# Optimization experiments

Measured on AMD Instinct MI355X. Metric: run time of the kernel, lower is better.

The kernel has to match this reference:

```python
import jax, jax.numpy as jnp
import numpy as np

B, H, SQ, SKV, D = 2, 16, 2048, 2048, 64
SCALE = 8  # sqrt(head_dim)


def setup_inputs() -> dict:
    key = jax.random.key(0)
    kq, kk, kv, km = jax.random.split(key, 4)
    q = jax.random.normal(kq, (B, H, SQ, D), dtype=jnp.float32)
    k = jax.random.normal(kk, (B, H, SKV, D), dtype=jnp.float32)
    v = jax.random.normal(kv, (B, H, SKV, D), dtype=jnp.float32)
    mask = jax.random.normal(km, (1, 1, SQ, SKV), dtype=jnp.float32)
    return {"q": q, "k": k, "v": v, "mask": mask, "scale": SCALE}


def reference(q, k, v, mask, scale):
    # scores: [B, H, SQ, SKV]
    scores = jnp.einsum("bhqd,bhkd->bhqk", q, k) / scale
    scores = scores + mask  # broadcast additive mask
    probs = jax.nn.softmax(scores, axis=-1)
    # hidden: [B, H, SQ, D]
    return jnp.einsum("bhqk,bhkd->bhqd", probs, v)
```

## Files before the change

kernel.cpp:

```cpp
#include <hip/hip_runtime.h>
#include <hip/hip_bf16.h>

#define NB 2
#define NH 16
#define NSQ 2048
#define NSKV 2048
#define ND 64
#define NT (NSKV / 64)
#define LOG2E 1.4426950408889634f

typedef __attribute__((ext_vector_type(8))) short bf16x8;
typedef __attribute__((ext_vector_type(4))) float f32x4;

__device__ __forceinline__ short f2bf(float x) {
  union { float f; unsigned u; } c; c.f = x;
  unsigned r = c.u + 0x7fffu + ((c.u >> 16) & 1u);
  return (short)(r >> 16);
}
__device__ __forceinline__ unsigned pack_bf2(float lo, float hi) {
  union { __hip_bfloat162 h; unsigned u; } c;
  c.h = __float22bfloat162_rn(float2{lo, hi});
  return c.u;
}
__device__ __forceinline__ float u2f(unsigned u) {
  union { unsigned u; float f; } c; c.u = u; return c.f;
}
__device__ __forceinline__ float exp2_fast(float x) {
#if __has_builtin(__builtin_amdgcn_exp2f)
  return __builtin_amdgcn_exp2f(x);
#else
  return exp2f(x);
#endif
}

__device__ __forceinline__ int kvmap(int x) {
  return (x & 3) | (((x >> 4) & 1) << 2) | (((x >> 2) & 1) << 3)
       | (((x >> 3) & 1) << 4) | (x & 32);
}

__global__ void prep_k(const float* __restrict__ K, short* __restrict__ Kp) {
  const int bh   = blockIdx.y;
  const int t    = (int)threadIdx.x;
  const int rout = blockIdx.x * 16 + (t >> 4);
  const int c    = (t & 15) * 4;
  const int rsrc = (rout & ~63) | kvmap(rout & 63);
  float4 v = *(const float4*)(K + ((size_t)bh * NSKV + rsrc) * ND + c);
  short4 o;
  o.x = f2bf(v.x); o.y = f2bf(v.y); o.z = f2bf(v.z); o.w = f2bf(v.w);
  *(short4*)(Kp + ((size_t)bh * NSKV + rout) * ND + c) = o;
}

__global__ void prep_vt(const float* __restrict__ V, short* __restrict__ Vt) {
  __shared__ float T[64][65];
  const int kv0 = blockIdx.x * 64;
  const int bh  = blockIdx.y;
  const int t   = (int)threadIdx.x;
  const float* src = V + ((size_t)bh * NSKV + kv0) * ND;
#pragma unroll
  for (int i = 0; i < 4; ++i) {
    float4 v = *(const float4*)(src + (size_t)((t >> 4) + 16 * i) * ND + (t & 15) * 4);
    T[(t >> 4) + 16 * i][(t & 15) * 4 + 0] = v.x;
    T[(t >> 4) + 16 * i][(t & 15) * 4 + 1] = v.y;
    T[(t >> 4) + 16 * i][(t & 15) * 4 + 2] = v.z;
    T[(t >> 4) + 16 * i][(t & 15) * 4 + 3] = v.w;
  }
  __syncthreads();
  const int d = t >> 2, kc = (t & 3) * 16;
  short* dst = Vt + ((size_t)bh * ND + d) * NSKV + kv0 + kc;
  bf16x8 w0, w1;
#pragma unroll
  for (int j = 0; j < 8; ++j) w0[j] = f2bf(T[kc + j][d]);
#pragma unroll
  for (int j = 0; j < 8; ++j) w1[j] = f2bf(T[kc + 8 + j][d]);
  *(bf16x8*)dst = w0;
  *(bf16x8*)(dst + 8) = w1;
}

__global__ void prep_mt(const float* __restrict__ M, unsigned short* __restrict__ Mt) {
  const int qt = blockIdx.x;
  const int kt = blockIdx.y;
  const int t  = (int)threadIdx.x;
  const int rl = t >> 4;
  const int c  = t & 15;
  const int row = qt * 16 + rl;
  float4 v = *(const float4*)(M + (size_t)row * NSKV + kt * 64 + c * 4);
  const int nt   = 2 * (c >> 3) + (c & 1);
  const int lq   = (c >> 1) & 3;
  const int lane = lq * 16 + rl;
  ushort4 o;
  o.x = (unsigned short)f2bf(LOG2E * v.x);
  o.y = (unsigned short)f2bf(LOG2E * v.y);
  o.z = (unsigned short)f2bf(LOG2E * v.z);
  o.w = (unsigned short)f2bf(LOG2E * v.w);
  *(ushort4*)(Mt + (((size_t)qt * 32 + kt) * 64 + lane) * 16 + nt * 4) = o;
}

__global__ __launch_bounds__(256, 2)
void attn_fwd(const float* __restrict__ Q, const short* __restrict__ Kbf,
              const short* __restrict__ Vt, const unsigned short* __restrict__ Mt,
              const void* __restrict__ scale_p, float* __restrict__ O)
{
  const int lin = (int)blockIdx.x + ((int)blockIdx.y << 4);
  const int swz = ((lin & 7) << 6) | (lin >> 3);
  const int qb  = swz & 15;
  const int bh  = swz >> 4;

  const int tid = (int)threadIdx.x;
  const int wv  = tid >> 6;
  const int ln  = tid & 63;
  const int l16 = ln & 15;
  const int lq  = ln >> 4;

  float scale_v;
  {
    union { int i; float f; } u;
    u.i = ((const int*)scale_p)[0];
    float af = fabsf(u.f);
    scale_v = (af >= 1e-6f && af <= 1e6f) ? u.f : (float)u.i;
  }
  const float qmul = LOG2E / scale_v;

  const int q0 = qb * 128;
  const short* Kg = Kbf + (size_t)bh * NSKV * ND;
  const short* Vg = Vt  + (size_t)bh * ND * NSKV;

  __shared__ short Kl[2][64][64];
  __shared__ short Vl[2][64][64];

  const int srow0  = tid >> 3;
  const int schunk = tid & 7;

  bf16x8 kst[2], vst[2];
#pragma unroll
  for (int j = 0; j < 2; ++j) {
    const int row = srow0 + j * 32;
    kst[j] = *(const bf16x8*)(Kg + (size_t)row * ND + schunk * 8);
    vst[j] = *(const bf16x8*)(Vg + (size_t)row * NSKV + schunk * 8);
  }

  bf16x8 qf[2][2];
  {
#pragma unroll
    for (int qs = 0; qs < 2; ++qs) {
      const float* qrow = Q + ((size_t)bh * NSQ + q0 + wv * 32 + qs * 16 + l16) * ND;
#pragma unroll
      for (int kc = 0; kc < 2; ++kc) {
        const float4* p = (const float4*)(qrow + kc * 32 + lq * 8);
        float4 a = p[0], b = p[1];
        bf16x8 f;
        f[0]=f2bf(a.x*qmul); f[1]=f2bf(a.y*qmul); f[2]=f2bf(a.z*qmul); f[3]=f2bf(a.w*qmul);
        f[4]=f2bf(b.x*qmul); f[5]=f2bf(b.y*qmul); f[6]=f2bf(b.z*qmul); f[7]=f2bf(b.w*qmul);
        qf[qs][kc] = f;
      }
    }
  }

  f32x4 oa[2][4];
  f32x4 lacc[2];
#pragma unroll
  for (int qs = 0; qs < 2; ++qs) {
#pragma unroll
    for (int dt = 0; dt < 4; ++dt) { f32x4 z = {0.f,0.f,0.f,0.f}; oa[qs][dt] = z; }
    f32x4 z = {0.f,0.f,0.f,0.f}; lacc[qs] = z;
  }

  bf16x8 ones;
#pragma unroll
  for (int j = 0; j < 8; ++j) ones[j] = (short)0x3F80;

  const unsigned short* Mq0 = Mt + ((size_t)(qb * 8 + wv * 2)) * 32 * 64 * 16 + (size_t)ln * 16;
  const unsigned short* Mq1 = Mq0 + (size_t)32 * 64 * 16;

  auto lds_write = [&](int buf) {
#pragma unroll
    for (int j = 0; j < 2; ++j) {
      const int row  = srow0 + j * 32;
      const int slot = schunk ^ (row & 7);
      *(bf16x8*)&Kl[buf][row][slot * 8] = kst[j];
      *(bf16x8*)&Vl[buf][row][slot * 8] = vst[j];
    }
  };

  union MU { uint4 q[2]; unsigned u[8]; };
  MU mc[2];

  lds_write(0);
  mc[0].q[0] = *(const uint4*)(Mq0);
  mc[0].q[1] = *(const uint4*)(Mq0 + 8);
  mc[1].q[0] = *(const uint4*)(Mq1);
  mc[1].q[1] = *(const uint4*)(Mq1 + 8);
  __syncthreads();

  for (int t = 0; t < NT; ++t) {
    const int cur = t & 1;
    const int kvb = t * 64;

    if (t + 1 < NT) {
#pragma unroll
      for (int j = 0; j < 2; ++j) {
        const int row = srow0 + j * 32;
        kst[j] = *(const bf16x8*)(Kg + (size_t)(kvb + 64 + row) * ND + schunk * 8);
        vst[j] = *(const bf16x8*)(Vg + (size_t)row * NSKV + kvb + 64 + schunk * 8);
      }
    }

    bf16x8 kf[4][2];
#pragma unroll
    for (int nt = 0; nt < 4; ++nt)
#pragma unroll
      for (int kc = 0; kc < 2; ++kc) {
        const int row = nt * 16 + l16;
        kf[nt][kc] = *(const bf16x8*)&Kl[cur][row][(((kc << 2) | lq) ^ (row & 7)) * 8];
      }

    f32x4 s0[4], s1[4];
    __builtin_amdgcn_s_setprio(1);
#pragma unroll
    for (int nt = 0; nt < 4; ++nt) {
      f32x4 a0 = {0.f,0.f,0.f,0.f};
      a0 = __builtin_amdgcn_mfma_f32_16x16x32_bf16(kf[nt][0], qf[0][0], a0, 0, 0, 0);
      a0 = __builtin_amdgcn_mfma_f32_16x16x32_bf16(kf[nt][1], qf[0][1], a0, 0, 0, 0);
      s0[nt] = a0;
      f32x4 a1 = {0.f,0.f,0.f,0.f};
      a1 = __builtin_amdgcn_mfma_f32_16x16x32_bf16(kf[nt][0], qf[1][0], a1, 0, 0, 0);
      a1 = __builtin_amdgcn_mfma_f32_16x16x32_bf16(kf[nt][1], qf[1][1], a1, 0, 0, 0);
      s1[nt] = a1;
    }
    __builtin_amdgcn_s_setprio(0);

    bf16x8 vfr[4][2];
#pragma unroll
    for (int dt = 0; dt < 4; ++dt)
#pragma unroll
      for (int kc = 0; kc < 2; ++kc) {
        const int row = dt * 16 + l16;
        vfr[dt][kc] = *(const bf16x8*)&Vl[cur][row][(((kc << 2) | lq) ^ (row & 7)) * 8];
      }

    {
#pragma unroll
      for (int nt = 0; nt < 4; ++nt) {
        const unsigned w0 = mc[0].u[nt * 2], w1 = mc[0].u[nt * 2 + 1];
        s0[nt][0] = exp2_fast(s0[nt][0] + u2f(w0 << 16));
        s0[nt][1] = exp2_fast(s0[nt][1] + u2f(w0 & 0xffff0000u));
        s0[nt][2] = exp2_fast(s0[nt][2] + u2f(w1 << 16));
        s0[nt][3] = exp2_fast(s0[nt][3] + u2f(w1 & 0xffff0000u));
      }
      bf16x8 pa[2];
#pragma unroll
      for (int kc = 0; kc < 2; ++kc) {
        union { unsigned u[4]; bf16x8 v; } w;
        w.u[0] = pack_bf2(s0[2*kc][0],   s0[2*kc][1]);
        w.u[1] = pack_bf2(s0[2*kc][2],   s0[2*kc][3]);
        w.u[2] = pack_bf2(s0[2*kc+1][0], s0[2*kc+1][1]);
        w.u[3] = pack_bf2(s0[2*kc+1][2], s0[2*kc+1][3]);
        pa[kc] = w.v;
      }
      __builtin_amdgcn_s_setprio(1);
#pragma unroll
      for (int kc = 0; kc < 2; ++kc) {
#pragma unroll
        for (int dt = 0; dt < 4; ++dt)
          oa[0][dt] = __builtin_amdgcn_mfma_f32_16x16x32_bf16(pa[kc], vfr[dt][kc], oa[0][dt], 0, 0, 0);
        lacc[0] = __builtin_amdgcn_mfma_f32_16x16x32_bf16(pa[kc], ones, lacc[0], 0, 0, 0);
      }
      __builtin_amdgcn_s_setprio(0);
    }

    {
#pragma unroll
      for (int nt = 0; nt < 4; ++nt) {
        const unsigned w0 = mc[1].u[nt * 2], w1 = mc[1].u[nt * 2 + 1];
        s1[nt][0] = exp2_fast(s1[nt][0] + u2f(w0 << 16));
        s1[nt][1] = exp2_fast(s1[nt][1] + u2f(w0 & 0xffff0000u));
        s1[nt][2] = exp2_fast(s1[nt][2] + u2f(w1 << 16));
        s1[nt][3] = exp2_fast(s1[nt][3] + u2f(w1 & 0xffff0000u));
      }
      if (t + 1 < NT) {
        const unsigned short* mp0 = Mq0 + (size_t)(t + 1) * 64 * 16;
        const unsigned short* mp1 = Mq1 + (size_t)(t + 1) * 64 * 16;
        mc[0].q[0] = *(const uint4*)(mp0);
        mc[0].q[1] = *(const uint4*)(mp0 + 8);
        mc[1].q[0] = *(const uint4*)(mp1);
        mc[1].q[1] = *(const uint4*)(mp1 + 8);
      }
      bf16x8 pa[2];
#pragma unroll
      for (int kc = 0; kc < 2; ++kc) {
        union { unsigned u[4]; bf16x8 v; } w;
        w.u[0] = pack_bf2(s1[2*kc][0],   s1[2*kc][1]);
        w.u[1] = pack_bf2(s1[2*kc][2],   s1[2*kc][3]);
        w.u[2] = pack_bf2(s1[2*kc+1][0], s1[2*kc+1][1]);
        w.u[3] = pack_bf2(s1[2*kc+1][2], s1[2*kc+1][3]);
        pa[kc] = w.v;
      }
      __builtin_amdgcn_s_setprio(1);
#pragma unroll
      for (int kc = 0; kc < 2; ++kc) {
#pragma unroll
        for (int dt = 0; dt < 4; ++dt)
          oa[1][dt] = __builtin_amdgcn_mfma_f32_16x16x32_bf16(pa[kc], vfr[dt][kc], oa[1][dt], 0, 0, 0);
        lacc[1] = __builtin_amdgcn_mfma_f32_16x16x32_bf16(pa[kc], ones, lacc[1], 0, 0, 0);
      }
      __builtin_amdgcn_s_setprio(0);
    }

    if (t + 1 < NT) lds_write(cur ^ 1);
    __syncthreads();
  }

#pragma unroll
  for (int qs = 0; qs < 2; ++qs)
#pragma unroll
    for (int r = 0; r < 4; ++r) {
      const float inv = 1.0f / lacc[qs][r];
      float* orow = O + ((size_t)bh * NSQ + q0 + wv * 32 + qs * 16 + lq * 4 + r) * ND;
#pragma unroll
      for (int dt = 0; dt < 4; ++dt)
        orow[dt * 16 + l16] = oa[qs][dt][r] * inv;
    }
}

extern "C" void kernel_launch(void* const* d_in, const int* in_sizes, int n_in,
                              void* d_out, int out_size, void* d_ws, size_t ws_size,
                              hipStream_t stream) {
  const float* q     = (const float*)d_in[0];
  const float* k     = (const float*)d_in[1];
  const float* v     = (const float*)d_in[2];
  const float* mask  = (const float*)d_in[3];
  const void*  scale = (const void*)d_in[4];
  float* out = (float*)d_out;

  const size_t NELEM = (size_t)NB * NH * NSKV * ND;
  short* Kbf = (short*)d_ws;
  short* Vtp = Kbf + NELEM;
  unsigned short* Mtl = (unsigned short*)(Vtp + NELEM);

  prep_k<<<dim3(NSKV / 16, NB * NH), 256, 0, stream>>>(k, Kbf);
  prep_vt<<<dim3(NSKV / 64, NB * NH), 256, 0, stream>>>(v, Vtp);
  prep_mt<<<dim3(NSQ / 16, NSKV / 64), 256, 0, stream>>>(mask, Mtl);

  dim3 grid(NSQ / 128, NB * NH);
  attn_fwd<<<grid, 256, 0, stream>>>(q, Kbf, Vtp, Mtl, scale, out);
}
```

Before: 73.70 us.

## Pre-pack K/V into MFMA fragment layout and load directly from global, dropping LDS

The prep kernels now write K and V in per-lane MFMA fragment order, so each lane loads its fragments with contiguous 16-byte global reads. This removes LDS staging, the swizzle and the per-tile __syncthreads. K fragments for the next tile are register-prefetched, and the two q-subtile QK/PV phases are interleaved to overlap exp work with MFMA. In exchange, every wave re-reads K/V from global/L2 instead of sharing them through LDS across four waves, and register pressure rises.

Measured after the change: 78.87 us. 1.07x slower.

```diff
diff --git a/kernel.cpp b/kernel.cpp
--- a/kernel.cpp
+++ b/kernel.cpp
@@ -8,6 +8,7 @@
 #define ND 64
 #define NT (NSKV / 64)
 #define LOG2E 1.4426950408889634f
+#define BHSTRIDE (NSKV * ND)
 
 typedef __attribute__((ext_vector_type(8))) short bf16x8;
 typedef __attribute__((ext_vector_type(4))) float f32x4;
@@ -39,18 +40,23 @@
 }
 
 __global__ void prep_k(const float* __restrict__ K, short* __restrict__ Kp) {
-  const int bh   = blockIdx.y;
-  const int t    = (int)threadIdx.x;
-  const int rout = blockIdx.x * 16 + (t >> 4);
-  const int c    = (t & 15) * 4;
-  const int rsrc = (rout & ~63) | kvmap(rout & 63);
-  float4 v = *(const float4*)(K + ((size_t)bh * NSKV + rsrc) * ND + c);
-  short4 o;
-  o.x = f2bf(v.x); o.y = f2bf(v.y); o.z = f2bf(v.z); o.w = f2bf(v.w);
-  *(short4*)(Kp + ((size_t)bh * NSKV + rout) * ND + c) = o;
-}
-
-__global__ void prep_vt(const float* __restrict__ V, short* __restrict__ Vt) {
+  const int bh = blockIdx.y, tile = blockIdx.x, tid = (int)threadIdx.x;
+#pragma unroll
+  for (int h = 0; h < 2; ++h) {
+    const int u    = tid + h * 256;
+    const int nt   = u >> 7, kc = (u >> 6) & 1, lane = u & 63;
+    const int prow = nt * 16 + (lane & 15);
+    const float* src = K + ((size_t)bh * NSKV + tile * 64 + kvmap(prow)) * ND
+                         + kc * 32 + (lane >> 4) * 8;
+    float4 a = *(const float4*)src, b = *(const float4*)(src + 4);
+    bf16x8 w;
+    w[0]=f2bf(a.x); w[1]=f2bf(a.y); w[2]=f2bf(a.z); w[3]=f2bf(a.w);
+    w[4]=f2bf(b.x); w[5]=f2bf(b.y); w[6]=f2bf(b.z); w[7]=f2bf(b.w);
+    *(bf16x8*)(Kp + (size_t)bh * BHSTRIDE + (size_t)tile * 4096 + u * 8) = w;
+  }
+}
+
+__global__ void prep_vt(const float* __restrict__ V, short* __restrict__ Vp) {
   __shared__ float T[64][65];
   const int kv0 = blockIdx.x * 64;
   const int bh  = blockIdx.y;
@@ -65,15 +71,18 @@
     T[(t >> 4) + 16 * i][(t & 15) * 4 + 3] = v.w;
   }
   __syncthreads();
-  const int d = t >> 2, kc = (t & 3) * 16;
-  short* dst = Vt + ((size_t)bh * ND + d) * NSKV + kv0 + kc;
+  const int d = t >> 2, c = t & 3;
   bf16x8 w0, w1;
 #pragma unroll
-  for (int j = 0; j < 8; ++j) w0[j] = f2bf(T[kc + j][d]);
-#pragma unroll
-  for (int j = 0; j < 8; ++j) w1[j] = f2bf(T[kc + 8 + j][d]);
-  *(bf16x8*)dst = w0;
-  *(bf16x8*)(dst + 8) = w1;
+  for (int j = 0; j < 8; ++j) w0[j] = f2bf(T[c * 16 + j][d]);
+#pragma unroll
+  for (int j = 0; j < 8; ++j) w1[j] = f2bf(T[c * 16 + 8 + j][d]);
+  const int frag  = (d >> 4) * 2 + (c >> 1);
+  const int lane0 = (((2 * c) & 3) << 4) | (d & 15);
+  const int lane1 = (((2 * c + 1) & 3) << 4) | (d & 15);
+  short* dstb = Vp + (size_t)bh * BHSTRIDE + (size_t)blockIdx.x * 4096 + frag * 512;
+  *(bf16x8*)(dstb + lane0 * 8) = w0;
+  *(bf16x8*)(dstb + lane1 * 8) = w1;
 }
 
 __global__ void prep_mt(const float* __restrict__ M, unsigned short* __restrict__ Mt) {
@@ -96,8 +105,8 @@
 }
 
 __global__ __launch_bounds__(256, 2)
-void attn_fwd(const float* __restrict__ Q, const short* __restrict__ Kbf,
-              const short* __restrict__ Vt, const unsigned short* __restrict__ Mt,
+void attn_fwd(const float* __restrict__ Q, const short* __restrict__ Kp,
+              const short* __restrict__ Vp, const unsigned short* __restrict__ Mt,
               const void* __restrict__ scale_p, float* __restrict__ O)
 {
   const int lin = (int)blockIdx.x + ((int)blockIdx.y << 4);
@@ -121,37 +130,21 @@
   const float qmul = LOG2E / scale_v;
 
   const int q0 = qb * 128;
-  const short* Kg = Kbf + (size_t)bh * NSKV * ND;
-  const short* Vg = Vt  + (size_t)bh * ND * NSKV;
-
-  __shared__ short Kl[2][64][64];
-  __shared__ short Vl[2][64][64];
-
-  const int srow0  = tid >> 3;
-  const int schunk = tid & 7;
-
-  bf16x8 kst[2], vst[2];
-#pragma unroll
-  for (int j = 0; j < 2; ++j) {
-    const int row = srow0 + j * 32;
-    kst[j] = *(const bf16x8*)(Kg + (size_t)row * ND + schunk * 8);
-    vst[j] = *(const bf16x8*)(Vg + (size_t)row * NSKV + schunk * 8);
-  }
+  const short* Kb = Kp + (size_t)bh * BHSTRIDE;
+  const short* Vb = Vp + (size_t)bh * BHSTRIDE;
 
   bf16x8 qf[2][2];
-  {
-#pragma unroll
-    for (int qs = 0; qs < 2; ++qs) {
-      const float* qrow = Q + ((size_t)bh * NSQ + q0 + wv * 32 + qs * 16 + l16) * ND;
-#pragma unroll
-      for (int kc = 0; kc < 2; ++kc) {
-        const float4* p = (const float4*)(qrow + kc * 32 + lq * 8);
-        float4 a = p[0], b = p[1];
-        bf16x8 f;
-        f[0]=f2bf(a.x*qmul); f[1]=f2bf(a.y*qmul); f[2]=f2bf(a.z*qmul); f[3]=f2bf(a.w*qmul);
-        f[4]=f2bf(b.x*qmul); f[5]=f2bf(b.y*qmul); f[6]=f2bf(b.z*qmul); f[7]=f2bf(b.w*qmul);
-        qf[qs][kc] = f;
-      }
+#pragma unroll
+  for (int qs = 0; qs < 2; ++qs) {
+    const float* qrow = Q + ((size_t)bh * NSQ + q0 + wv * 32 + qs * 16 + l16) * ND;
+#pragma unroll
+    for (int kc = 0; kc < 2; ++kc) {
+      const float4* p = (const float4*)(qrow + kc * 32 + lq * 8);
+      float4 a = p[0], b = p[1];
+      bf16x8 f;
+      f[0]=f2bf(a.x*qmul); f[1]=f2bf(a.y*qmul); f[2]=f2bf(a.z*qmul); f[3]=f2bf(a.w*qmul);
+      f[4]=f2bf(b.x*qmul); f[5]=f2bf(b.y*qmul); f[6]=f2bf(b.z*qmul); f[7]=f2bf(b.w*qmul);
+      qf[qs][kc] = f;
     }
   }
 
@@ -171,72 +164,50 @@
   const unsigned short* Mq0 = Mt + ((size_t)(qb * 8 + wv * 2)) * 32 * 64 * 16 + (size_t)ln * 16;
   const unsigned short* Mq1 = Mq0 + (size_t)32 * 64 * 16;
 
-  auto lds_write = [&](int buf) {
-#pragma unroll
-    for (int j = 0; j < 2; ++j) {
-      const int row  = srow0 + j * 32;
-      const int slot = schunk ^ (row & 7);
-      *(bf16x8*)&Kl[buf][row][slot * 8] = kst[j];
-      *(bf16x8*)&Vl[buf][row][slot * 8] = vst[j];
-    }
-  };
-
   union MU { uint4 q[2]; unsigned u[8]; };
-  MU mc[2];
-
-  lds_write(0);
+  MU mc[2], mn[2];
+
+  bf16x8 kfc[4][2], kfn[4][2], vf[4][2];
+#pragma unroll
+  for (int nt = 0; nt < 4; ++nt)
+#pragma unroll
+    for (int kc = 0; kc < 2; ++kc)
+      kfc[nt][kc] = *(const bf16x8*)(Kb + (nt * 2 + kc) * 512 + ln * 8);
   mc[0].q[0] = *(const uint4*)(Mq0);
   mc[0].q[1] = *(const uint4*)(Mq0 + 8);
   mc[1].q[0] = *(const uint4*)(Mq1);
   mc[1].q[1] = *(const uint4*)(Mq1 + 8);
-  __syncthreads();
-
+
+#pragma unroll 2
   for (int t = 0; t < NT; ++t) {
-    const int cur = t & 1;
-    const int kvb = t * 64;
+    const short* Vt0 = Vb + (size_t)t * 4096;
+#pragma unroll
+    for (int dt = 0; dt < 4; ++dt)
+#pragma unroll
+      for (int kc = 0; kc < 2; ++kc)
+        vf[dt][kc] = *(const bf16x8*)(Vt0 + (dt * 2 + kc) * 512 + ln * 8);
 
     if (t + 1 < NT) {
-#pragma unroll
-      for (int j = 0; j < 2; ++j) {
-        const int row = srow0 + j * 32;
-        kst[j] = *(const bf16x8*)(Kg + (size_t)(kvb + 64 + row) * ND + schunk * 8);
-        vst[j] = *(const bf16x8*)(Vg + (size_t)row * NSKV + kvb + 64 + schunk * 8);
-      }
-    }
-
-    bf16x8 kf[4][2];
-#pragma unroll
-    for (int nt = 0; nt < 4; ++nt)
-#pragma unroll
-      for (int kc = 0; kc < 2; ++kc) {
-        const int row = nt * 16 + l16;
-        kf[nt][kc] = *(const bf16x8*)&Kl[cur][row][(((kc << 2) | lq) ^ (row & 7)) * 8];
-      }
-
-    f32x4 s0[4], s1[4];
+      const short* Kt1 = Kb + (size_t)(t + 1) * 4096;
+#pragma unroll
+      for (int nt = 0; nt < 4; ++nt)
+#pragma unroll
+        for (int kc = 0; kc < 2; ++kc)
+          kfn[nt][kc] = *(const bf16x8*)(Kt1 + (nt * 2 + kc) * 512 + ln * 8);
+    }
+
+    f32x4 s0[4];
     __builtin_amdgcn_s_setprio(1);
 #pragma unroll
     for (int nt = 0; nt < 4; ++nt) {
-      f32x4 a0 = {0.f,0.f,0.f,0.f};
-      a0 = __builtin_amdgcn_mfma_f32_16x16x32_bf16(kf[nt][0], qf[0][0], a0, 0, 0, 0);
-      a0 = __builtin_amdgcn_mfma_f32_16x16x32_bf16(kf[nt][1], qf[0][1], a0, 0, 0, 0);
-      s0[nt] = a0;
-      f32x4 a1 = {0.f,0.f,0.f,0.f};
-      a1 = __builtin_amdgcn_mfma_f32_16x16x32_bf16(kf[nt][0], qf[1][0], a1, 0, 0, 0);
-      a1 = __builtin_amdgcn_mfma_f32_16x16x32_bf16(kf[nt][1], qf[1][1], a1, 0, 0, 0);
-      s1[nt] = a1;
+      f32x4 a = {0.f,0.f,0.f,0.f};
+      a = __builtin_amdgcn_mfma_f32_16x16x32_bf16(kfc[nt][0], qf[0][0], a, 0, 0, 0);
+      a = __builtin_amdgcn_mfma_f32_16x16x32_bf16(kfc[nt][1], qf[0][1], a, 0, 0, 0);
+      s0[nt] = a;
     }
     __builtin_amdgcn_s_setprio(0);
 
-    bf16x8 vfr[4][2];
-#pragma unroll
-    for (int dt = 0; dt < 4; ++dt)
-#pragma unroll
-      for (int kc = 0; kc < 2; ++kc) {
-        const int row = dt * 16 + l16;
-        vfr[dt][kc] = *(const bf16x8*)&Vl[cur][row][(((kc << 2) | lq) ^ (row & 7)) * 8];
-      }
-
+    bf16x8 pa0[2];
     {
 #pragma unroll
       for (int nt = 0; nt < 4; ++nt) {
@@ -246,7 +217,6 @@
         s0[nt][2] = exp2_fast(s0[nt][2] + u2f(w1 << 16));
         s0[nt][3] = exp2_fast(s0[nt][3] + u2f(w1 & 0xffff0000u));
       }
-      bf16x8 pa[2];
 #pragma unroll
       for (int kc = 0; kc < 2; ++kc) {
         union { unsigned u[4]; bf16x8 v; } w;
@@ -254,19 +224,41 @@
         w.u[1] = pack_bf2(s0[2*kc][2],   s0[2*kc][3]);
         w.u[2] = pack_bf2(s0[2*kc+1][0], s0[2*kc+1][1]);
         w.u[3] = pack_bf2(s0[2*kc+1][2], s0[2*kc+1][3]);
-        pa[kc] = w.v;
+        pa0[kc] = w.v;
       }
-      __builtin_amdgcn_s_setprio(1);
-#pragma unroll
-      for (int kc = 0; kc < 2; ++kc) {
-#pragma unroll
-        for (int dt = 0; dt < 4; ++dt)
-          oa[0][dt] = __builtin_amdgcn_mfma_f32_16x16x32_bf16(pa[kc], vfr[dt][kc], oa[0][dt], 0, 0, 0);
-        lacc[0] = __builtin_amdgcn_mfma_f32_16x16x32_bf16(pa[kc], ones, lacc[0], 0, 0, 0);
-      }
-      __builtin_amdgcn_s_setprio(0);
-    }
-
+    }
+
+    f32x4 s1[4];
+    __builtin_amdgcn_s_setprio(1);
+#pragma unroll
+    for (int nt = 0; nt < 4; ++nt) {
+      f32x4 a = {0.f,0.f,0.f,0.f};
+      a = __builtin_amdgcn_mfma_f32_16x16x32_bf16(kfc[nt][0], qf[1][0], a, 0, 0, 0);
+      a = __builtin_amdgcn_mfma_f32_16x16x32_bf16(kfc[nt][1], qf[1][1], a, 0, 0, 0);
+      s1[nt] = a;
+    }
+    __builtin_amdgcn_s_setprio(0);
+
+    if (t + 1 < NT) {
+      const unsigned short* mp0 = Mq0 + (size_t)(t + 1) * 64 * 16;
+      const unsigned short* mp1 = Mq1 + (size_t)(t + 1) * 64 * 16;
+      mn[0].q[0] = *(const uint4*)(mp0);
+      mn[0].q[1] = *(const uint4*)(mp0 + 8);
+      mn[1].q[0] = *(const uint4*)(mp1);
+      mn[1].q[1] = *(const uint4*)(mp1 + 8);
+    }
+
+    __builtin_amdgcn_s_setprio(1);
+#pragma unroll
+    for (int kc = 0; kc < 2; ++kc) {
+#pragma unroll
+      for (int dt = 0; dt < 4; ++dt)
+        oa[0][dt] = __builtin_amdgcn_mfma_f32_16x16x32_bf16(pa0[kc], vf[dt][kc], oa[0][dt], 0, 0, 0);
+      lacc[0] = __builtin_amdgcn_mfma_f32_16x16x32_bf16(pa0[kc], ones, lacc[0], 0, 0, 0);
+    }
+    __builtin_amdgcn_s_setprio(0);
+
+    bf16x8 pa1[2];
     {
 #pragma unroll
       for (int nt = 0; nt < 4; ++nt) {
@@ -276,15 +268,6 @@
         s1[nt][2] = exp2_fast(s1[nt][2] + u2f(w1 << 16));
         s1[nt][3] = exp2_fast(s1[nt][3] + u2f(w1 & 0xffff0000u));
       }
-      if (t + 1 < NT) {
-        const unsigned short* mp0 = Mq0 + (size_t)(t + 1) * 64 * 16;
-        const unsigned short* mp1 = Mq1 + (size_t)(t + 1) * 64 * 16;
-        mc[0].q[0] = *(const uint4*)(mp0);
-        mc[0].q[1] = *(const uint4*)(mp0 + 8);
-        mc[1].q[0] = *(const uint4*)(mp1);
-        mc[1].q[1] = *(const uint4*)(mp1 + 8);
-      }
-      bf16x8 pa[2];
 #pragma unroll
       for (int kc = 0; kc < 2; ++kc) {
         union { unsigned u[4]; bf16x8 v; } w;
@@ -292,21 +275,27 @@
         w.u[1] = pack_bf2(s1[2*kc][2],   s1[2*kc][3]);
         w.u[2] = pack_bf2(s1[2*kc+1][0], s1[2*kc+1][1]);
         w.u[3] = pack_bf2(s1[2*kc+1][2], s1[2*kc+1][3]);
-        pa[kc] = w.v;
+        pa1[kc] = w.v;
       }
-      __builtin_amdgcn_s_setprio(1);
-#pragma unroll
-      for (int kc = 0; kc < 2; ++kc) {
-#pragma unroll
-        for (int dt = 0; dt < 4; ++dt)
-          oa[1][dt] = __builtin_amdgcn_mfma_f32_16x16x32_bf16(pa[kc], vfr[dt][kc], oa[1][dt], 0, 0, 0);
-        lacc[1] = __builtin_amdgcn_mfma_f32_16x16x32_bf16(pa[kc], ones, lacc[1], 0, 0, 0);
-      }
-      __builtin_amdgcn_s_setprio(0);
-    }
-
-    if (t + 1 < NT) lds_write(cur ^ 1);
-    __syncthreads();
+    }
+
+    __builtin_amdgcn_s_setprio(1);
+#pragma unroll
+    for (int kc = 0; kc < 2; ++kc) {
+#pragma unroll
+      for (int dt = 0; dt < 4; ++dt)
+        oa[1][dt] = __builtin_amdgcn_mfma_f32_16x16x32_bf16(pa1[kc], vf[dt][kc], oa[1][dt], 0, 0, 0);
+      lacc[1] = __builtin_amdgcn_mfma_f32_16x16x32_bf16(pa1[kc], ones, lacc[1], 0, 0, 0);
+    }
+    __builtin_amdgcn_s_setprio(0);
+
+#pragma unroll
+    for (int nt = 0; nt < 4; ++nt)
+#pragma unroll
+      for (int kc = 0; kc < 2; ++kc)
+        kfc[nt][kc] = kfn[nt][kc];
+    mc[0] = mn[0];
+    mc[1] = mn[1];
   }
 
 #pragma unroll
@@ -332,14 +321,14 @@
   float* out = (float*)d_out;
 
   const size_t NELEM = (size_t)NB * NH * NSKV * ND;
-  short* Kbf = (short*)d_ws;
-  short* Vtp = Kbf + NELEM;
-  unsigned short* Mtl = (unsigned short*)(Vtp + NELEM);
-
-  prep_k<<<dim3(NSKV / 16, NB * NH), 256, 0, stream>>>(k, Kbf);
-  prep_vt<<<dim3(NSKV / 64, NB * NH), 256, 0, stream>>>(v, Vtp);
+  short* Kpk = (short*)d_ws;
+  short* Vpk = Kpk + NELEM;
+  unsigned short* Mtl = (unsigned short*)(Vpk + NELEM);
+
+  prep_k<<<dim3(NSKV / 64, NB * NH), 256, 0, stream>>>(k, Kpk);
+  prep_vt<<<dim3(NSKV / 64, NB * NH), 256, 0, stream>>>(v, Vpk);
   prep_mt<<<dim3(NSQ / 16, NSKV / 64), 256, 0, stream>>>(mask, Mtl);
 
   dim3 grid(NSQ / 128, NB * NH);
-  attn_fwd<<<grid, 256, 0, stream>>>(q, Kbf, Vtp, Mtl, scale, out);
-}
+  attn_fwd<<<grid, 256, 0, stream>>>(q, Kpk, Vpk, Mtl, scale, out);
+}
```
